# Kernel tuning notes

Measured on AMD Instinct MI355X. Metric: run time of the kernel, lower is better.

The kernel has to match this reference:

```python
import math
import jax, jax.numpy as jnp
import numpy as np

T_STEPS = 128       # number of diffusion 'experts'
BASE = 64
CH = BASE * 2       # 128 working channels
TE = 256            # time embedding dim
B, IN_C, H, W = 8, 3, 128, 128
EPS = 1e-5


def _conv(x, w, b):
    # x: [N,C,H,W], w: [O,I,3,3] (or 1x1)
    y = jax.lax.conv_general_dilated(x, w, (1, 1), 'SAME',
                                     dimension_numbers=('NCHW', 'OIHW', 'NCHW'))
    return y + b[None, :, None, None]


def _gn(x, scale, bias, groups=8):
    n, c, h, w = x.shape
    xg = x.reshape(n, groups, c // groups, h, w)
    m = xg.mean((2, 3, 4), keepdims=True)
    v = xg.var((2, 3, 4), keepdims=True)
    xn = ((xg - m) * jax.lax.rsqrt(v + EPS)).reshape(n, c, h, w)
    return xn * scale[None, :, None, None] + bias[None, :, None, None]


def setup_inputs() -> dict:
    key = jax.random.key(0)
    ks = iter(jax.random.split(key, 64))
    def p(shape, s=0.05):
        return jax.random.normal(next(ks), shape, jnp.float32) * s
    return {
        'x': jax.random.normal(next(ks), (B, IN_C, H, W), jnp.float32),
        't': jax.random.randint(next(ks), (B,), 0, T_STEPS),
        # feature_extraction
        'fe_w1': p((BASE, IN_C, 3, 3)), 'fe_b1': jnp.zeros((BASE,), jnp.float32),
        'fe_g1s': jnp.ones((BASE,), jnp.float32), 'fe_g1b': jnp.zeros((BASE,), jnp.float32),
        'fe_w2': p((CH, BASE, 3, 3)), 'fe_b2': jnp.zeros((CH,), jnp.float32),
        'fe_g2s': jnp.ones((CH,), jnp.float32), 'fe_g2b': jnp.zeros((CH,), jnp.float32),
        # stacked per-step expert params [T, ...]
        'mlp_w1': p((T_STEPS, TE, TE)), 'mlp_b1': jnp.zeros((T_STEPS, TE), jnp.float32),
        'mlp_w2': p((T_STEPS, CH, TE)), 'mlp_b2': jnp.zeros((T_STEPS, CH), jnp.float32),
        'c1w': p((T_STEPS, CH, CH + 1, 3, 3)), 'c1b': jnp.zeros((T_STEPS, CH), jnp.float32),
        'g1s': jnp.ones((T_STEPS, CH), jnp.float32), 'g1b': jnp.zeros((T_STEPS, CH), jnp.float32),
        'c2w': p((T_STEPS, CH, CH, 3, 3)), 'c2b': jnp.zeros((T_STEPS, CH), jnp.float32),
        'g2s': jnp.ones((T_STEPS, CH), jnp.float32), 'g2b': jnp.zeros((T_STEPS, CH), jnp.float32),
        'c3w': p((T_STEPS, CH, CH, 3, 3)), 'c3b': jnp.zeros((T_STEPS, CH), jnp.float32),
        # color_reconstruction
        'cr_w1': p((BASE, CH, 3, 3)), 'cr_b1': jnp.zeros((BASE,), jnp.float32),
        'cr_gs': jnp.ones((BASE,), jnp.float32), 'cr_gb': jnp.zeros((BASE,), jnp.float32),
        'cr_w2': p((IN_C, BASE, 3, 3)), 'cr_b2': jnp.zeros((IN_C,), jnp.float32),
        # weight_generator (1x1 conv on pooled features)
        'wg_w': p((1, CH, 1, 1)), 'wg_b': jnp.zeros((1,), jnp.float32),
    }


def _expert(xi, tei, w1, b1, w2, b2, cw1, cb1, gs1, gb1, cw2, cb2, gs2, gb2, cw3, cb3):
    # Single-sample DiffusionStep. xi: [C,H,W], tei: [TE]
    h = jax.nn.silu(w1 @ tei + b1)
    tc = (w2 @ h + b2).mean()  # scalar time channel (fix of original view(-1,1,1,1) bug)
    xb = xi[None]  # [1,C,H,W]
    tmap = jnp.broadcast_to(tc, (1, 1) + xi.shape[1:])
    z = jnp.concatenate([xb, tmap], axis=1)  # [1,C+1,H,W]
    z = jax.nn.silu(_gn(_conv(z, cw1, cb1), gs1, gb1))
    z = jax.nn.silu(_gn(_conv(z, cw2, cb2), gs2, gb2))
    z = _conv(z, cw3, cb3)
    return z[0]


def _forward(x, t, fe_w1, fe_b1, fe_g1s, fe_g1b, fe_w2, fe_b2, fe_g2s, fe_g2b,
             mlp_w1, mlp_b1, mlp_w2, mlp_b2, c1w, c1b, g1s, g1b,
             c2w, c2b, g2s, g2b, c3w, c3b,
             cr_w1, cr_b1, cr_gs, cr_gb, cr_w2, cr_b2, wg_w, wg_b):
    feat = jax.nn.silu(_gn(_conv(x, fe_w1, fe_b1), fe_g1s, fe_g1b))
    feat = jax.nn.silu(_gn(_conv(feat, fe_w2, fe_b2), fe_g2s, fe_g2b))  # [B,CH,H,W]

    # sinusoidal time embedding
    half = TE // 2
    freqs = jnp.exp(jnp.arange(half, dtype=jnp.float32) * (-math.log(10000.0) / (half - 1)))
    e = t.astype(jnp.float32)[:, None] * freqs[None, :]
    temb = jnp.concatenate([jnp.sin(e), jnp.cos(e)], axis=-1)  # [B,TE]

    # Each sample matches exactly one step: gather its expert weights, apply once.
    g = lambda a: jnp.take(a, t, axis=0)
    noise = jax.vmap(_expert)(feat, temb,
                              g(mlp_w1), g(mlp_b1), g(mlp_w2), g(mlp_b2),
                              g(c1w), g(c1b), g(g1s), g(g1b),
                              g(c2w), g(c2b), g(g2s), g(g2b),
                              g(c3w), g(c3b))
    alpha = 1.0 - t.astype(jnp.float32) / T_STEPS
    x_t = feat - alpha[:, None, None, None] * noise

    r = jax.nn.silu(_gn(_conv(x_t, cr_w1, cr_b1), cr_gs, cr_gb))
    restored = jax.nn.sigmoid(_conv(r, cr_w2, cr_b2))  # [B,3,H,W]

    pooled = x_t.mean((2, 3))  # adaptive avg pool to 1x1 -> [B,CH]
    weight = jax.nn.sigmoid(pooled @ wg_w[:, :, 0, 0].T + wg_b)[:, :, None, None]  # [B,1,1,1]
    return restored, weight


def reference(x, t, fe_w1, fe_b1, fe_g1s, fe_g1b, fe_w2, fe_b2, fe_g2s, fe_g2b,
              mlp_w1, mlp_b1, mlp_w2, mlp_b2, c1w, c1b, g1s, g1b,
              c2w, c2b, g2s, g2b, c3w, c3b,
              cr_w1, cr_b1, cr_gs, cr_gb, cr_w2, cr_b2, wg_w, wg_b):
    return _forward(x, t, fe_w1, fe_b1, fe_g1s, fe_g1b, fe_w2, fe_b2, fe_g2s, fe_g2b,
                    mlp_w1, mlp_b1, mlp_w2, mlp_b2, c1w, c1b, g1s, g1b,
                    c2w, c2b, g2s, g2b, c3w, c3b,
                    cr_w1, cr_b1, cr_gs, cr_gb, cr_w2, cr_b2, wg_w, wg_b)
```

## Files before the change

kernel.cpp:

```cpp
#include <hip/hip_runtime.h>
#include <hip/hip_bf16.h>

typedef __hip_bfloat16 bf16;

#define HW 128
#define IMG 16384
#define EPSV 1e-5f

typedef __bf16 b16x8 __attribute__((ext_vector_type(8)));
typedef float f32x16 __attribute__((ext_vector_type(16)));

__device__ __forceinline__ float u2f(unsigned int u){ union{unsigned int i; float f;}c; c.i=u; return c.f; }
__device__ __forceinline__ float blo(unsigned int u){ return u2f(u<<16); }
__device__ __forceinline__ float bhi(unsigned int u){ return u2f(u & 0xffff0000u); }
__device__ __forceinline__ unsigned short f2bu(float v){ bf16 h=__float2bfloat16(v); union{bf16 b; unsigned short s;}c; c.b=h; return c.s; }
__device__ __forceinline__ unsigned int pk(float a, float b){ return (unsigned int)f2bu(a) | ((unsigned int)f2bu(b)<<16); }
__device__ __forceinline__ bf16 f2b(float v){ return __float2bfloat16(v); }
__device__ __forceinline__ float sigm(float x){ return 1.f/(1.f+__expf(-x)); }

__device__ __forceinline__ void gload16(const void* g, void* l) {
    __builtin_amdgcn_global_load_lds((const __attribute__((address_space(1))) unsigned int*)(g),
                                     (__attribute__((address_space(3))) unsigned int*)(l), 16, 0, 0);
}

__device__ __forceinline__ f32x16 MFMA(b16x8 a, b16x8 b, f32x16 c){
    return __builtin_amdgcn_mfma_f32_32x32x16_bf16(a, b, c, 0, 0, 0);
}

template<int CIN, int COUT, bool TADD>
__global__ void __launch_bounds__(256, 2)
mfma_conv3x3(const bf16* __restrict__ act,
             const bf16* __restrict__ Wt,
             const float* __restrict__ Bt,
             bf16* __restrict__ outp,
             const float* __restrict__ Tt,
             const bf16* __restrict__ zerobuf)
{
    static_assert(CIN==64 || CIN==128, "");
    static_assert(COUT==64 || COUT==128, "");
    constexpr int NT = COUT/64;
    constexpr int XB_ROW = 136*128;
    constexpr int XB_BYTES = 2*XB_ROW;
    constexpr int WA_BYTES = COUT*128;
    __shared__ char smem[XB_BYTES + WA_BYTES];
    char* Xb = smem;
    char* Wa = smem + XB_BYTES;

    const int n    = blockIdx.z;
    const int tile = blockIdx.x;
    const int y0   = tile*2;
    const int tid  = threadIdx.x;
    const int lane = tid & 63;
    const int wid  = tid >> 6;
    const int wm   = wid >> 1;
    const int wn   = wid & 1;
    const int l31  = lane & 31;
    const int lhi  = lane >> 5;

    const bf16* actN = act + (size_t)n * IMG * CIN;
    const bf16* WtN  = Wt  + (size_t)n * 9 * COUT * CIN;

    f32x16 acc[4][NT];
    #pragma unroll
    for (int i=0;i<4;++i)
        #pragma unroll
        for (int j=0;j<NT;++j)
            #pragma unroll
            for (int k=0;k<16;++k) acc[i][j][k] = 0.f;

    for (int dy = 0; dy < 3; ++dy) {
        for (int ch = 0; ch < CIN/64; ++ch) {
            for (int u = wid; u < 34; u += 4) {
                int row  = (u >= 17) ? 1 : 0;
                int j    = u - row*17;
                int slot = j*64 + lane;
                int xp = slot >> 3, g = slot & 7;
                int x  = xp - 1;
                int ry = y0 + dy - 1 + row;
                const void* src;
                if ((unsigned)x < 128u && (unsigned)ry < 128u)
                    src = actN + ((size_t)(ry*128 + x)*CIN + ch*64 + 8*(g ^ (xp&7)));
                else
                    src = zerobuf;
                gload16(src, Xb + row*XB_ROW + j*1024);
            }
            for (int dx = 0; dx < 3; ++dx) {
                int r = dy*3 + dx;
                for (int u = wid; u < COUT/8; u += 4) {
                    int co = u*8 + (lane>>3), g = lane & 7;
                    const void* src = WtN + ((size_t)(r*COUT + co)*CIN + ch*64 + 8*(g ^ (co&7)));
                    gload16(src, Wa + u*1024);
                }
                __syncthreads();
                #pragma unroll
                for (int s = 0; s < 4; ++s) {
                    int koff = s*32 + lhi*16;
                    b16x8 bfr[NT];
                    #pragma unroll
                    for (int q = 0; q < NT; ++q) {
                        int co = wn*32*NT + q*32 + l31;
                        bfr[q] = *(const b16x8*)(Wa + co*128 + (koff ^ ((co&7)<<4)));
                    }
                    b16x8 afr[4];
                    #pragma unroll
                    for (int mt = 0; mt < 4; ++mt) {
                        int xp = mt*32 + l31 + dx;
                        afr[mt] = *(const b16x8*)(Xb + wm*XB_ROW + xp*128 + (koff ^ ((xp&7)<<4)));
                    }
                    #pragma unroll
                    for (int mt = 0; mt < 4; ++mt)
                        #pragma unroll
                        for (int q = 0; q < NT; ++q)
                            acc[mt][q] = MFMA(afr[mt], bfr[q], acc[mt][q]);
                }
                __syncthreads();
            }
        }
    }

    const float* BtN = Bt + n*COUT;
    const int y = y0 + wm;
    bf16* outRow = outp + ((size_t)n*IMG + (size_t)y*128)*COUT;
    #pragma unroll
    for (int q = 0; q < NT; ++q) {
        int co = wn*32*NT + q*32 + l31;
        float bv = BtN[co];
        float T0=0.f, T1=0.f, T2=0.f;
        if (TADD) {
            int yt = (y==0) ? 0 : (y==127 ? 2 : 1);
            const float* Tp = Tt + (size_t)(n*COUT + co)*9 + yt*3;
            T0 = Tp[0]; T1 = Tp[1]; T2 = Tp[2];
        }
        #pragma unroll
        for (int mt = 0; mt < 4; ++mt) {
            #pragma unroll
            for (int reg = 0; reg < 16; ++reg) {
                int x = mt*32 + (reg&3) + 8*(reg>>2) + 4*lhi;
                float v = acc[mt][q][reg] + bv;
                if (TADD) v += (x==0) ? T0 : (x==127 ? T2 : T1);
                outRow[(size_t)x*COUT + co] = f2b(v);
            }
        }
    }
}

__global__ void __launch_bounds__(256)
wtprep_kernel(const float* __restrict__ w, const float* __restrict__ b,
              const int* __restrict__ t, bf16* __restrict__ Wt, float* __restrict__ Bt,
              int CO, int COsrc, int CIN, int CINW, int gather)
{
    int idx = blockIdx.x*256 + threadIdx.x;
    int total = 8*9*CO*CIN;
    if (idx >= total) return;
    int cin = idx & (CIN-1);
    int tmp = idx / CIN;
    int co  = tmp % CO;
    int tmp2 = tmp / CO;
    int r   = tmp2 % 9;
    int n   = tmp2 / 9;
    int sel = gather ? t[n] : 0;
    float v = 0.f;
    if (co < COsrc) v = w[(((size_t)sel*COsrc + co)*CINW + cin)*9 + r];
    Wt[idx] = f2b(v);
    if (cin==0 && r==0) Bt[n*CO+co] = (co < COsrc) ? b[(size_t)sel*COsrc + co] : 0.f;
}

__global__ void __launch_bounds__(256)
tprep_kernel(const int* __restrict__ t, const float* __restrict__ c1w,
             const float* __restrict__ tc, float* __restrict__ Tt)
{
    int idx = blockIdx.x*256 + threadIdx.x;
    if (idx >= 8*128) return;
    int n = idx >> 7, co = idx & 127;
    const float* wp = c1w + ((size_t)t[n]*128 + co)*129*9 + 128*9;
    float w9[9];
    #pragma unroll
    for (int i=0;i<9;++i) w9[i] = wp[i];
    float tcv = tc[n];
    #pragma unroll
    for (int yt=0; yt<3; ++yt)
        #pragma unroll
        for (int xt=0; xt<3; ++xt) {
            float s = 0.f;
            #pragma unroll
            for (int dy=0; dy<3; ++dy)
                #pragma unroll
                for (int dx=0; dx<3; ++dx) {
                    bool vy = (yt==0) ? (dy>=1) : ((yt==2) ? (dy<=1) : true);
                    bool vx = (xt==0) ? (dx>=1) : ((xt==2) ? (dx<=1) : true);
                    if (vy && vx) s += w9[dy*3+dx];
                }
            Tt[(size_t)idx*9 + yt*3+xt] = tcv*s;
        }
}

__global__ void __launch_bounds__(256)
fe1_kernel(const float* __restrict__ in, const float* __restrict__ w,
           const float* __restrict__ bias, bf16* __restrict__ out)
{
    const int n   = blockIdx.z;
    const int co0 = blockIdx.y * 8;
    const int tx0 = (blockIdx.x & 7) * 16;
    const int ty0 = (blockIdx.x >> 3) * 16;
    const int lx = threadIdx.x & 15, ly = threadIdx.x >> 4;
    __shared__ float tileS[18][19];
    float acc[8];
    #pragma unroll
    for (int i=0;i<8;++i) acc[i] = bias[co0+i];
    const float* inN = in + (size_t)n*3*IMG;
    for (int ci=0; ci<3; ++ci) {
        __syncthreads();
        for (int idx = threadIdx.x; idx < 18*18; idx += 256) {
            int tyy = idx/18, txx = idx - tyy*18;
            int gy = ty0+tyy-1, gx = tx0+txx-1;
            float v = 0.f;
            if ((unsigned)gy < 128u && (unsigned)gx < 128u) v = inN[ci*IMG + gy*128+gx];
            tileS[tyy][txx] = v;
        }
        __syncthreads();
        float v[9];
        #pragma unroll
        for (int ky=0;ky<3;++ky)
            #pragma unroll
            for (int kx=0;kx<3;++kx) v[ky*3+kx] = tileS[ly+ky][lx+kx];
        #pragma unroll
        for (int c=0;c<8;++c) {
            const float* wp = w + ((co0+c)*3 + ci)*9;
            #pragma unroll
            for (int k=0;k<9;++k) acc[c] = fmaf(v[k], wp[k], acc[c]);
        }
    }
    int gy = ty0+ly, gx = tx0+lx;
    uint4 o; o.x = pk(acc[0],acc[1]); o.y = pk(acc[2],acc[3]);
    o.z = pk(acc[4],acc[5]); o.w = pk(acc[6],acc[7]);
    *(uint4*)(out + ((size_t)n*IMG + gy*128+gx)*64 + co0) = o;
}

template<int C>
__global__ void __launch_bounds__(256)
gn_stats_nhwc(const bf16* __restrict__ x, float* __restrict__ partials)
{
    constexpr int L2CPG = (C==128) ? 4 : 3;
    const int chunk = blockIdx.x, n = blockIdx.y;
    const int t = threadIdx.x;
    const uint4* pv = (const uint4*)(x + ((size_t)n*IMG + chunk*256 + t)*C);
    float s[8], ss[8];
    #pragma unroll
    for (int g=0; g<8; ++g) { s[g]=0.f; ss[g]=0.f; }
    #pragma unroll
    for (int v=0; v<C/8; ++v) {
        int g = (v*8) >> L2CPG;
        uint4 u = pv[v];
        float f0=blo(u.x), f1=bhi(u.x), f2=blo(u.y), f3=bhi(u.y);
        float f4=blo(u.z), f5=bhi(u.z), f6=blo(u.w), f7=bhi(u.w);
        s[g]  += ((f0+f1)+(f2+f3)) + ((f4+f5)+(f6+f7));
        ss[g] += ((f0*f0+f1*f1)+(f2*f2+f3*f3)) + ((f4*f4+f5*f5)+(f6*f6+f7*f7));
    }
    __shared__ float sh[16][256];
    #pragma unroll
    for (int g=0; g<8; ++g) { sh[2*g][t] = s[g]; sh[2*g+1][t] = ss[g]; }
    __syncthreads();
    for (int off=128; off>0; off>>=1) {
        if (t < off) {
            #pragma unroll
            for (int k=0;k<16;++k) sh[k][t] += sh[k][t+off];
        }
        __syncthreads();
    }
    if (t < 16) partials[((size_t)n*64 + chunk)*16 + t] = sh[t][0];
}

__global__ void __launch_bounds__(128)
gn_final(const float* __restrict__ partials, const float* __restrict__ scale,
         const float* __restrict__ bias, const int* __restrict__ tsel,
         int C, int l2cpg, float* __restrict__ scA, float* __restrict__ biA)
{
    int n = blockIdx.x, c = threadIdx.x;
    if (c >= C) return;
    int g = c >> l2cpg;
    float s=0.f, ss=0.f;
    for (int k=0;k<64;++k) {
        s  += partials[((size_t)n*64+k)*16 + 2*g];
        ss += partials[((size_t)n*64+k)*16 + 2*g + 1];
    }
    float cnt = (float)IMG * (float)(C>>3);
    float m = s/cnt, var = ss/cnt - m*m;
    float r = rsqrtf(var + EPSV);
    int po = tsel ? tsel[n]*C : 0;
    float sc = scale[po+c]*r;
    scA[n*C+c] = sc;
    biA[n*C+c] = bias[po+c] - m*sc;
}

template<int C>
__global__ void __launch_bounds__(256)
gn_apply_nhwc(bf16* __restrict__ x, const float* __restrict__ scA, const float* __restrict__ biA)
{
    size_t e0 = ((size_t)blockIdx.x*256 + threadIdx.x)*8;
    int n = (int)(e0 >> ((C==128) ? 21 : 20));
    int c0 = (int)(e0 & (C-1));
    const float4 sA = *(const float4*)(scA + n*C + c0);
    const float4 sB = *(const float4*)(scA + n*C + c0 + 4);
    const float4 bA = *(const float4*)(biA + n*C + c0);
    const float4 bB = *(const float4*)(biA + n*C + c0 + 4);
    uint4* p = (uint4*)(x + e0);
    uint4 u = *p;
    float f[8] = {blo(u.x),bhi(u.x),blo(u.y),bhi(u.y),blo(u.z),bhi(u.z),blo(u.w),bhi(u.w)};
    f[0]=f[0]*sA.x+bA.x; f[1]=f[1]*sA.y+bA.y; f[2]=f[2]*sA.z+bA.z; f[3]=f[3]*sA.w+bA.w;
    f[4]=f[4]*sB.x+bB.x; f[5]=f[5]*sB.y+bB.y; f[6]=f[6]*sB.z+bB.z; f[7]=f[7]*sB.w+bB.w;
    #pragma unroll
    for (int i=0;i<8;++i) f[i] = f[i]*sigm(f[i]);
    u.x = pk(f[0],f[1]); u.y = pk(f[2],f[3]); u.z = pk(f[4],f[5]); u.w = pk(f[6],f[7]);
    *p = u;
}

__global__ void __launch_bounds__(256)
time_mlp_kernel(const int* __restrict__ t,
                const float* __restrict__ w1, const float* __restrict__ b1,
                const float* __restrict__ w2, const float* __restrict__ b2,
                float* __restrict__ tc)
{
    const int n = blockIdx.x;
    const int ti = t[n];
    const int tid = threadIdx.x;
    __shared__ float temb[256];
    __shared__ float h[256];
    {
        int j = tid & 127;
        float fr = expf(-9.210340371976184f / 127.f * (float)j);
        float e = (float)ti * fr;
        temb[tid] = (tid < 128) ? sinf(e) : cosf(e);
    }
    __syncthreads();
    {
        const float* w1p = w1 + ((size_t)ti * 256 + tid) * 256;
        float s = b1[(size_t)ti * 256 + tid];
        for (int j = 0; j < 256; ++j) s += w1p[j] * temb[j];
        h[tid] = s * sigm(s);
    }
    __syncthreads();
    float part = 0.f;
    if (tid < 128) {
        const float* w2p = w2 + ((size_t)ti * 128 + tid) * 256;
        float s = b2[(size_t)ti * 128 + tid];
        for (int j = 0; j < 256; ++j) s += w2p[j] * h[j];
        part = s;
    }
    __shared__ float red[256];
    red[tid] = part;
    __syncthreads();
    for (int off = 128; off > 0; off >>= 1) {
        if (tid < off) red[tid] += red[tid + off];
        __syncthreads();
    }
    if (tid == 0) tc[n] = red[0] * (1.f / 128.f);
}

__global__ void __launch_bounds__(256)
xt_pool_nhwc(bf16* __restrict__ feat, const bf16* __restrict__ noise,
             const int* __restrict__ t, const float* __restrict__ wgw,
             float* __restrict__ partials)
{
    size_t e0 = ((size_t)blockIdx.x*256 + threadIdx.x)*8;
    int n = (int)(e0 >> 21);
    int c0 = (int)(e0 & 127);
    float alpha = 1.f - (float)t[n] * (1.f / 128.f);
    const float4 wA = *(const float4*)(wgw + c0);
    const float4 wB = *(const float4*)(wgw + c0 + 4);
    uint4 f = *(const uint4*)(feat + e0);
    uint4 z = *(const uint4*)(noise + e0);
    float xf[8] = {blo(f.x),bhi(f.x),blo(f.y),bhi(f.y),blo(f.z),bhi(f.z),blo(f.w),bhi(f.w)};
    float xz[8] = {blo(z.x),bhi(z.x),blo(z.y),bhi(z.y),blo(z.z),bhi(z.z),blo(z.w),bhi(z.w)};
    float wv[8] = {wA.x,wA.y,wA.z,wA.w,wB.x,wB.y,wB.z,wB.w};
    float s = 0.f;
    #pragma unroll
    for (int i=0;i<8;++i) { float v = xf[i] - alpha*xz[i]; xf[i] = v; s += v*wv[i]; }
    uint4 o;
    o.x = pk(xf[0],xf[1]); o.y = pk(xf[2],xf[3]); o.z = pk(xf[4],xf[5]); o.w = pk(xf[6],xf[7]);
    *(uint4*)(feat + e0) = o;
    __shared__ float sh[256];
    sh[threadIdx.x] = s;
    __syncthreads();
    for (int off = 128; off > 0; off >>= 1) {
        if ((int)threadIdx.x < off) sh[threadIdx.x] += sh[threadIdx.x + off];
        __syncthreads();
    }
    if (threadIdx.x == 0) partials[blockIdx.x] = sh[0];
}

__global__ void __launch_bounds__(256)
weight_final_kernel(const float* __restrict__ partials, const float* __restrict__ wg_b,
                    float* __restrict__ outw)
{
    const int n = blockIdx.x;
    float s = 0.f;
    for (int i = threadIdx.x; i < 1024; i += 256) s += partials[n * 1024 + i];
    __shared__ float sh[256];
    sh[threadIdx.x] = s;
    __syncthreads();
    for (int off = 128; off > 0; off >>= 1) {
        if ((int)threadIdx.x < off) sh[threadIdx.x] += sh[threadIdx.x + off];
        __syncthreads();
    }
    if (threadIdx.x == 0) {
        float w = sh[0] * (1.f / 16384.f) + wg_b[0];
        outw[n] = sigm(w);
    }
}

__global__ void __launch_bounds__(256)
extract_kernel(const bf16* __restrict__ in, float* __restrict__ out)
{
    int n = blockIdx.y;
    int px = blockIdx.x*256 + threadIdx.x;
    const bf16* p = in + ((size_t)n*IMG + px)*64;
    float r0 = __bfloat162float(p[0]);
    float r1 = __bfloat162float(p[1]);
    float r2 = __bfloat162float(p[2]);
    size_t ob = (size_t)n*3*IMG + px;
    out[ob]         = sigm(r0);
    out[ob + IMG]   = sigm(r1);
    out[ob + 2*IMG] = sigm(r2);
}

extern "C" void kernel_launch(void* const* d_in, const int* in_sizes, int n_in,
                              void* d_out, int out_size, void* d_ws, size_t ws_size,
                              hipStream_t stream)
{
    (void)in_sizes; (void)n_in; (void)out_size; (void)ws_size;

    const float* x      = (const float*)d_in[0];
    const int*   t      = (const int*)  d_in[1];
    const float* fe_w1  = (const float*)d_in[2];
    const float* fe_b1  = (const float*)d_in[3];
    const float* fe_g1s = (const float*)d_in[4];
    const float* fe_g1b = (const float*)d_in[5];
    const float* fe_w2  = (const float*)d_in[6];
    const float* fe_b2  = (const float*)d_in[7];
    const float* fe_g2s = (const float*)d_in[8];
    const float* fe_g2b = (const float*)d_in[9];
    const float* mlp_w1 = (const float*)d_in[10];
    const float* mlp_b1 = (const float*)d_in[11];
    const float* mlp_w2 = (const float*)d_in[12];
    const float* mlp_b2 = (const float*)d_in[13];
    const float* c1w    = (const float*)d_in[14];
    const float* c1b    = (const float*)d_in[15];
    const float* g1s    = (const float*)d_in[16];
    const float* g1b    = (const float*)d_in[17];
    const float* c2w    = (const float*)d_in[18];
    const float* c2b    = (const float*)d_in[19];
    const float* g2s    = (const float*)d_in[20];
    const float* g2b    = (const float*)d_in[21];
    const float* c3w    = (const float*)d_in[22];
    const float* c3b    = (const float*)d_in[23];
    const float* cr_w1  = (const float*)d_in[24];
    const float* cr_b1  = (const float*)d_in[25];
    const float* cr_gs  = (const float*)d_in[26];
    const float* cr_gb  = (const float*)d_in[27];
    const float* cr_w2  = (const float*)d_in[28];
    const float* cr_b2  = (const float*)d_in[29];
    const float* wg_w   = (const float*)d_in[30];
    const float* wg_b   = (const float*)d_in[31];

    char* ws = (char*)d_ws;
    bf16* A   = (bf16*)(ws);
    bf16* Bb  = (bf16*)(ws + 33554432);
    bf16* Cb  = (bf16*)(ws + 67108864);
    bf16* Wt  = (bf16*)(ws + 100663296);
    float* Bt = (float*)(ws + 103022592);
    float* Tt = (float*)(ws + 103026688);
    float* tc = (float*)(ws + 103063552);
    bf16* zb  = (bf16*)(ws + 103063616);
    float* gp = (float*)(ws + 103063680);
    float* scA = (float*)(ws + 103096448);
    float* biA = (float*)(ws + 103100544);
    float* wp  = (float*)(ws + 103104640);

    float* out_img = (float*)d_out;
    float* out_w   = out_img + 393216;

    dim3 blk(256);
    hipMemsetAsync(zb, 0, 64, stream);

    time_mlp_kernel<<<8, blk, 0, stream>>>(t, mlp_w1, mlp_b1, mlp_w2, mlp_b2, tc);
    tprep_kernel<<<4, blk, 0, stream>>>(t, c1w, tc, Tt);

    fe1_kernel<<<dim3(64, 8, 8), blk, 0, stream>>>(x, fe_w1, fe_b1, Bb);
    gn_stats_nhwc<64><<<dim3(64, 8), blk, 0, stream>>>(Bb, gp);
    gn_final<<<8, 128, 0, stream>>>(gp, fe_g1s, fe_g1b, nullptr, 64, 3, scA, biA);
    gn_apply_nhwc<64><<<4096, blk, 0, stream>>>(Bb, scA, biA);

    wtprep_kernel<<<2304, blk, 0, stream>>>(fe_w2, fe_b2, t, Wt, Bt, 128, 128, 64, 64, 0);
    mfma_conv3x3<64,128,false><<<dim3(64, 1, 8), blk, 0, stream>>>(Bb, Wt, Bt, A, nullptr, zb);
    gn_stats_nhwc<128><<<dim3(64, 8), blk, 0, stream>>>(A, gp);
    gn_final<<<8, 128, 0, stream>>>(gp, fe_g2s, fe_g2b, nullptr, 128, 4, scA, biA);
    gn_apply_nhwc<128><<<8192, blk, 0, stream>>>(A, scA, biA);

    wtprep_kernel<<<4608, blk, 0, stream>>>(c1w, c1b, t, Wt, Bt, 128, 128, 128, 129, 1);
    mfma_conv3x3<128,128,true><<<dim3(64, 1, 8), blk, 0, stream>>>(A, Wt, Bt, Bb, Tt, zb);
    gn_stats_nhwc<128><<<dim3(64, 8), blk, 0, stream>>>(Bb, gp);
    gn_final<<<8, 128, 0, stream>>>(gp, g1s, g1b, t, 128, 4, scA, biA);
    gn_apply_nhwc<128><<<8192, blk, 0, stream>>>(Bb, scA, biA);

    wtprep_kernel<<<4608, blk, 0, stream>>>(c2w, c2b, t, Wt, Bt, 128, 128, 128, 128, 1);
    mfma_conv3x3<128,128,false><<<dim3(64, 1, 8), blk, 0, stream>>>(Bb, Wt, Bt, Cb, nullptr, zb);
    gn_stats_nhwc<128><<<dim3(64, 8), blk, 0, stream>>>(Cb, gp);
    gn_final<<<8, 128, 0, stream>>>(gp, g2s, g2b, t, 128, 4, scA, biA);
    gn_apply_nhwc<128><<<8192, blk, 0, stream>>>(Cb, scA, biA);

    wtprep_kernel<<<4608, blk, 0, stream>>>(c3w, c3b, t, Wt, Bt, 128, 128, 128, 128, 1);
    mfma_conv3x3<128,128,false><<<dim3(64, 1, 8), blk, 0, stream>>>(Cb, Wt, Bt, Bb, nullptr, zb);

    xt_pool_nhwc<<<8192, blk, 0, stream>>>(A, Bb, t, wg_w, wp);
    weight_final_kernel<<<8, blk, 0, stream>>>(wp, wg_b, out_w);

    wtprep_kernel<<<2304, blk, 0, stream>>>(cr_w1, cr_b1, t, Wt, Bt, 64, 64, 128, 128, 0);
    mfma_conv3x3<128,64,false><<<dim3(64, 1, 8), blk, 0, stream>>>(A, Wt, Bt, Cb, nullptr, zb);
    gn_stats_nhwc<64><<<dim3(64, 8), blk, 0, stream>>>(Cb, gp);
    gn_final<<<8, 128, 0, stream>>>(gp, cr_gs, cr_gb, nullptr, 64, 3, scA, biA);
    gn_apply_nhwc<64><<<4096, blk, 0, stream>>>(Cb, scA, biA);

    wtprep_kernel<<<1152, blk, 0, stream>>>(cr_w2, cr_b2, t, Wt, Bt, 64, 3, 64, 64, 0);
    mfma_conv3x3<64,64,false><<<dim3(64, 1, 8), blk, 0, stream>>>(Cb, Wt, Bt, Bb, nullptr, zb);
    extract_kernel<<<dim3(64, 8), blk, 0, stream>>>(Bb, out_img);
}
```

Before: 443.8 us.

## Fuse GroupNorm stats and x_t/pool into conv epilogue, double-buffer weight staging

Each conv kernel now accumulates per-group sum and sum-of-squares in its epilogue and writes per-tile partials, which removes the separate gn_stats passes. The final expert conv computes x_t = feat - alpha*noise and the gating dot product in its epilogue, which removes the xt_pool kernel. The conv main loop is restructured to double-buffer weight tiles so the next tap's weights are prefetched while MFMA runs, with a compact input row layout and a raised wave priority during MFMA. The fused epilogues add register pressure and extra syncs, and the GN partial layout must still match what gn_final expects.

```diff
diff --git a/kernel.cpp b/kernel.cpp
--- a/kernel.cpp
+++ b/kernel.cpp
@@ -27,24 +27,31 @@
     return __builtin_amdgcn_mfma_f32_32x32x16_bf16(a, b, c, 0, 0, 0);
 }
 
-template<int CIN, int COUT, bool TADD>
+template<int CIN, int COUT, bool TADD, bool FUSE_GN, bool FUSE_XT>
 __global__ void __launch_bounds__(256, 2)
 mfma_conv3x3(const bf16* __restrict__ act,
              const bf16* __restrict__ Wt,
              const float* __restrict__ Bt,
              bf16* __restrict__ outp,
              const float* __restrict__ Tt,
-             const bf16* __restrict__ zerobuf)
+             const bf16* __restrict__ zerobuf,
+             float* __restrict__ gpart,
+             const bf16* __restrict__ featA,
+             const int* __restrict__ tsel,
+             const float* __restrict__ wgw,
+             float* __restrict__ wpart)
 {
     static_assert(CIN==64 || CIN==128, "");
     static_assert(COUT==64 || COUT==128, "");
-    constexpr int NT = COUT/64;
-    constexpr int XB_ROW = 136*128;
-    constexpr int XB_BYTES = 2*XB_ROW;
-    constexpr int WA_BYTES = COUT*128;
-    __shared__ char smem[XB_BYTES + WA_BYTES];
-    char* Xb = smem;
-    char* Wa = smem + XB_BYTES;
+    constexpr int NT  = COUT/64;
+    constexpr int CH  = CIN/64;
+    constexpr int P   = 9*CH;
+    constexpr int WCH = COUT/8;
+    constexpr int WSZ = WCH*1024;
+
+    __shared__ char Xb[33792];
+    __shared__ char Wa[2][WSZ];
+    __shared__ float redS[4][4], redSS[4][4], redW[4];
 
     const int n    = blockIdx.z;
     const int tile = blockIdx.x;
@@ -68,63 +75,107 @@
             #pragma unroll
             for (int k=0;k<16;++k) acc[i][j][k] = 0.f;
 
-    for (int dy = 0; dy < 3; ++dy) {
-        for (int ch = 0; ch < CIN/64; ++ch) {
-            for (int u = wid; u < 34; u += 4) {
-                int row  = (u >= 17) ? 1 : 0;
-                int j    = u - row*17;
-                int slot = j*64 + lane;
-                int xp = slot >> 3, g = slot & 7;
-                int x  = xp - 1;
-                int ry = y0 + dy - 1 + row;
-                const void* src;
-                if ((unsigned)x < 128u && (unsigned)ry < 128u)
-                    src = actN + ((size_t)(ry*128 + x)*CIN + ch*64 + 8*(g ^ (xp&7)));
-                else
-                    src = zerobuf;
-                gload16(src, Xb + row*XB_ROW + j*1024);
+    auto stage_X = [&](int dy, int ch) {
+        const int ry0 = y0 + dy - 1;
+        for (int u = wid; u < 33; u += 4) {
+            int s = u*8 + (lane>>3);
+            int g = lane & 7;
+            int r  = (s >= 130) ? 1 : 0;
+            int xp = s - r*130;
+            int xx = xp - 1;
+            int ry = ry0 + r;
+            const void* src = zerobuf;
+            if (s < 260 && (unsigned)xx < 128u && (unsigned)ry < 128u)
+                src = actN + ((size_t)(ry*128 + xx)*CIN + ch*64 + 8*(g ^ (s&7)));
+            gload16(src, Xb + u*1024);
+        }
+    };
+    auto stage_W = [&](int r, int ch, int buf) {
+        for (int u = wid; u < WCH; u += 4) {
+            int co = u*8 + (lane>>3);
+            int g  = lane & 7;
+            const void* src = WtN + ((size_t)(r*COUT + co)*CIN + ch*64 + 8*(g ^ (co&7)));
+            gload16(src, Wa[buf] + u*1024);
+        }
+    };
+
+    stage_X(0, 0);
+    stage_W(0, 0, 0);
+    __syncthreads();
+
+    int buf = 0;
+    for (int p = 0; p < P; ++p) {
+        const int dx = p % 3;
+        const int pc = p / 3;
+        const int ch = pc % CH;
+        const int dy = pc / CH;
+        const bool last = (p+1 == P);
+
+        if (!last) {
+            const int pn  = p + 1;
+            const int ndx = pn % 3;
+            const int npc = pn / 3;
+            const int nch = npc % CH;
+            const int ndy = npc / CH;
+            stage_W(ndy*3 + ndx, nch, buf ^ 1);
+        }
+        (void)dy; (void)ch;
+
+        __builtin_amdgcn_s_setprio(1);
+        #pragma unroll
+        for (int s = 0; s < 4; ++s) {
+            const int koff = s*32 + lhi*16;
+            b16x8 bfr[NT];
+            #pragma unroll
+            for (int q = 0; q < NT; ++q) {
+                int co = wn*32*NT + q*32 + l31;
+                bfr[q] = *(const b16x8*)(Wa[buf] + co*128 + (koff ^ ((co&7)<<4)));
             }
-            for (int dx = 0; dx < 3; ++dx) {
-                int r = dy*3 + dx;
-                for (int u = wid; u < COUT/8; u += 4) {
-                    int co = u*8 + (lane>>3), g = lane & 7;
-                    const void* src = WtN + ((size_t)(r*COUT + co)*CIN + ch*64 + 8*(g ^ (co&7)));
-                    gload16(src, Wa + u*1024);
-                }
+            b16x8 afr[4];
+            #pragma unroll
+            for (int mt = 0; mt < 4; ++mt) {
+                int sl = wm*130 + mt*32 + l31 + dx;
+                afr[mt] = *(const b16x8*)(Xb + sl*128 + (koff ^ ((sl&7)<<4)));
+            }
+            #pragma unroll
+            for (int mt = 0; mt < 4; ++mt)
+                #pragma unroll
+                for (int q = 0; q < NT; ++q)
+                    acc[mt][q] = MFMA(afr[mt], bfr[q], acc[mt][q]);
+        }
+        __builtin_amdgcn_s_setprio(0);
+
+        if (!last) {
+            if (dx == 2) {
                 __syncthreads();
-                #pragma unroll
-                for (int s = 0; s < 4; ++s) {
-                    int koff = s*32 + lhi*16;
-                    b16x8 bfr[NT];
-                    #pragma unroll
-                    for (int q = 0; q < NT; ++q) {
-                        int co = wn*32*NT + q*32 + l31;
-                        bfr[q] = *(const b16x8*)(Wa + co*128 + (koff ^ ((co&7)<<4)));
-                    }
-                    b16x8 afr[4];
-                    #pragma unroll
-                    for (int mt = 0; mt < 4; ++mt) {
-                        int xp = mt*32 + l31 + dx;
-                        afr[mt] = *(const b16x8*)(Xb + wm*XB_ROW + xp*128 + (koff ^ ((xp&7)<<4)));
-                    }
-                    #pragma unroll
-                    for (int mt = 0; mt < 4; ++mt)
-                        #pragma unroll
-                        for (int q = 0; q < NT; ++q)
-                            acc[mt][q] = MFMA(afr[mt], bfr[q], acc[mt][q]);
-                }
+                const int pn  = p + 1;
+                const int npc = pn / 3;
+                stage_X(npc / CH, npc % CH);
+                __syncthreads();
+            } else {
                 __syncthreads();
             }
         }
+        buf ^= 1;
     }
 
     const float* BtN = Bt + n*COUT;
     const int y = y0 + wm;
     bf16* outRow = outp + ((size_t)n*IMG + (size_t)y*128)*COUT;
+    const bf16* featRow = FUSE_XT ? (featA + ((size_t)n*IMG + (size_t)y*128)*COUT) : nullptr;
+    float alpha = 0.f;
+    if (FUSE_XT) alpha = 1.f - (float)tsel[n] * (1.f/128.f);
+
+    float gs[NT], gss[NT], wsum = 0.f;
+    #pragma unroll
+    for (int q = 0; q < NT; ++q) { gs[q]=0.f; gss[q]=0.f; }
+
     #pragma unroll
     for (int q = 0; q < NT; ++q) {
-        int co = wn*32*NT + q*32 + l31;
-        float bv = BtN[co];
+        const int co = wn*32*NT + q*32 + l31;
+        const float bv = BtN[co];
+        float wg = 0.f;
+        if (FUSE_XT) wg = wgw[co];
         float T0=0.f, T1=0.f, T2=0.f;
         if (TADD) {
             int yt = (y==0) ? 0 : (y==127 ? 2 : 1);
@@ -135,12 +186,52 @@
         for (int mt = 0; mt < 4; ++mt) {
             #pragma unroll
             for (int reg = 0; reg < 16; ++reg) {
-                int x = mt*32 + (reg&3) + 8*(reg>>2) + 4*lhi;
+                const int x = mt*32 + (reg&3) + 8*(reg>>2) + 4*lhi;
                 float v = acc[mt][q][reg] + bv;
                 if (TADD) v += (x==0) ? T0 : (x==127 ? T2 : T1);
-                outRow[(size_t)x*COUT + co] = f2b(v);
+                if (FUSE_GN) { gs[q] += v; gss[q] += v*v; }
+                if (FUSE_XT) {
+                    float fv = __bfloat162float(featRow[(size_t)x*COUT + co]);
+                    float xt = fv - alpha*v;
+                    outRow[(size_t)x*COUT + co] = f2b(xt);
+                    wsum += xt * wg;
+                } else {
+                    outRow[(size_t)x*COUT + co] = f2b(v);
+                }
             }
         }
+    }
+
+    if (FUSE_GN) {
+        constexpr int LG = (COUT==128) ? 4 : 3;
+        #pragma unroll
+        for (int q = 0; q < NT; ++q) {
+            float a = gs[q], b = gss[q];
+            #pragma unroll
+            for (int m = 1; m < (1<<LG); m <<= 1) { a += __shfl_xor(a, m); b += __shfl_xor(b, m); }
+            a += __shfl_xor(a, 32); b += __shfl_xor(b, 32);
+            const int co = wn*32*NT + q*32 + l31;
+            if (lhi == 0 && (l31 & ((1<<LG)-1)) == 0) {
+                int j = (co >> LG) & 3;
+                redS[wid][j] = a; redSS[wid][j] = b;
+            }
+        }
+        __syncthreads();
+        if (tid < 8) {
+            int g = tid, wn_ = g>>2, j = g&3;
+            float S  = redS[wn_][j]  + redS[2+wn_][j];
+            float SS = redSS[wn_][j] + redSS[2+wn_][j];
+            gpart[((size_t)(n*64 + tile))*16 + 2*g]     = S;
+            gpart[((size_t)(n*64 + tile))*16 + 2*g + 1] = SS;
+        }
+    }
+    if (FUSE_XT) {
+        float a = wsum;
+        #pragma unroll
+        for (int m = 1; m < 64; m <<= 1) a += __shfl_xor(a, m);
+        if (lane == 0) redW[wid] = a;
+        __syncthreads();
+        if (tid == 0) wpart[n*64 + tile] = redW[0]+redW[1]+redW[2]+redW[3];
     }
 }
 
@@ -356,56 +447,15 @@
     if (tid == 0) tc[n] = red[0] * (1.f / 128.f);
 }
 
-__global__ void __launch_bounds__(256)
-xt_pool_nhwc(bf16* __restrict__ feat, const bf16* __restrict__ noise,
-             const int* __restrict__ t, const float* __restrict__ wgw,
-             float* __restrict__ partials)
-{
-    size_t e0 = ((size_t)blockIdx.x*256 + threadIdx.x)*8;
-    int n = (int)(e0 >> 21);
-    int c0 = (int)(e0 & 127);
-    float alpha = 1.f - (float)t[n] * (1.f / 128.f);
-    const float4 wA = *(const float4*)(wgw + c0);
-    const float4 wB = *(const float4*)(wgw + c0 + 4);
-    uint4 f = *(const uint4*)(feat + e0);
-    uint4 z = *(const uint4*)(noise + e0);
-    float xf[8] = {blo(f.x),bhi(f.x),blo(f.y),bhi(f.y),blo(f.z),bhi(f.z),blo(f.w),bhi(f.w)};
-    float xz[8] = {blo(z.x),bhi(z.x),blo(z.y),bhi(z.y),blo(z.z),bhi(z.z),blo(z.w),bhi(z.w)};
-    float wv[8] = {wA.x,wA.y,wA.z,wA.w,wB.x,wB.y,wB.z,wB.w};
-    float s = 0.f;
-    #pragma unroll
-    for (int i=0;i<8;++i) { float v = xf[i] - alpha*xz[i]; xf[i] = v; s += v*wv[i]; }
-    uint4 o;
-    o.x = pk(xf[0],xf[1]); o.y = pk(xf[2],xf[3]); o.z = pk(xf[4],xf[5]); o.w = pk(xf[6],xf[7]);
-    *(uint4*)(feat + e0) = o;
-    __shared__ float sh[256];
-    sh[threadIdx.x] = s;
-    __syncthreads();
-    for (int off = 128; off > 0; off >>= 1) {
-        if ((int)threadIdx.x < off) sh[threadIdx.x] += sh[threadIdx.x + off];
-        __syncthreads();
-    }
-    if (threadIdx.x == 0) partials[blockIdx.x] = sh[0];
-}
-
-__global__ void __launch_bounds__(256)
-weight_final_kernel(const float* __restrict__ partials, const float* __restrict__ wg_b,
+__global__ void __launch_bounds__(64)
+weight_final_kernel(const float* __restrict__ wpart, const float* __restrict__ wg_b,
                     float* __restrict__ outw)
 {
     const int n = blockIdx.x;
-    float s = 0.f;
-    for (int i = threadIdx.x; i < 1024; i += 256) s += partials[n * 1024 + i];
-    __shared__ float sh[256];
-    sh[threadIdx.x] = s;
-    __syncthreads();
-    for (int off = 128; off > 0; off >>= 1) {
-        if ((int)threadIdx.x < off) sh[threadIdx.x] += sh[threadIdx.x + off];
-        __syncthreads();
-    }
-    if (threadIdx.x == 0) {
-        float w = sh[0] * (1.f / 16384.f) + wg_b[0];
-        outw[n] = sigm(w);
-    }
+    float s = wpart[n*64 + threadIdx.x];
+    #pragma unroll
+    for (int m = 1; m < 64; m <<= 1) s += __shfl_xor(s, m);
+    if (threadIdx.x == 0) outw[n] = sigm(s * (1.f/16384.f) + wg_b[0]);
 }
 
 __global__ void __launch_bounds__(256)
@@ -480,6 +530,7 @@
     float* out_w   = out_img + 393216;
 
     dim3 blk(256);
+    dim3 cgrid(64, 1, 8);
     hipMemsetAsync(zb, 0, 64, stream);
 
     time_mlp_kernel<<<8, blk, 0, stream>>>(t, mlp_w1, mlp_b1, mlp_w2, mlp_b2, tc);
@@ -491,36 +542,30 @@
     gn_apply_nhwc<64><<<4096, blk, 0, stream>>>(Bb, scA, biA);
 
     wtprep_kernel<<<2304, blk, 0, stream>>>(fe_w2, fe_b2, t, Wt, Bt, 128, 128, 64, 64, 0);
-    mfma_conv3x3<64,128,false><<<dim3(64, 1, 8), blk, 0, stream>>>(Bb, Wt, Bt, A, nullptr, zb);
-    gn_stats_nhwc<128><<<dim3(64, 8), blk, 0, stream>>>(A, gp);
+    mfma_conv3x3<64,128,false,true,false><<<cgrid, blk, 0, stream>>>(Bb, Wt, Bt, A, nullptr, zb, gp, nullptr, nullptr, nullptr, nullptr);
     gn_final<<<8, 128, 0, stream>>>(gp, fe_g2s, fe_g2b, nullptr, 128, 4, scA, biA);
     gn_apply_nhwc<128><<<8192, blk, 0, stream>>>(A, scA, biA);
 
     wtprep_kernel<<<4608, blk, 0, stream>>>(c1w, c1b, t, Wt, Bt, 128, 128, 128, 129, 1);
-    mfma_conv3x3<128,128,true><<<dim3(64, 1, 8), blk, 0, stream>>>(A, Wt, Bt, Bb, Tt, zb);
-    gn_stats_nhwc<128><<<dim3(64, 8), blk, 0, stream>>>(Bb, gp);
+    mfma_conv3x3<128,128,true,true,false><<<cgrid, blk, 0, stream>>>(A, Wt, Bt, Bb, Tt, zb, gp, nullptr, nullptr, nullptr, nullptr);
     gn_final<<<8, 128, 0, stream>>>(gp, g1s, g1b, t, 128, 4, scA, biA);
     gn_apply_nhwc<128><<<8192, blk, 0, stream>>>(Bb, scA, biA);
 
     wtprep_kernel<<<4608, blk, 0, stream>>>(c2w, c2b, t, Wt, Bt, 128, 128, 128, 128, 1);
-    mfma_conv3x3<128,128,false><<<dim3(64, 1, 8), blk, 0, stream>>>(Bb, Wt, Bt, Cb, nullptr, zb);
-    gn_stats_nhwc<128><<<dim3(64, 8), blk, 0, stream>>>(Cb, gp);
+    mfma_conv3x3<128,128,false,true,false><<<cgrid, blk, 0, stream>>>(Bb, Wt, Bt, Cb, nullptr, zb, gp, nullptr, nullptr, nullptr, nullptr);
     gn_final<<<8, 128, 0, stream>>>(gp, g2s, g2b, t, 128, 4, scA, biA);
     gn_apply_nhwc<128><<<8192, blk, 0, stream>>>(Cb, scA, biA);
 
     wtprep_kernel<<<4608, blk, 0, stream>>>(c3w, c3b, t, Wt, Bt, 128, 128, 128, 128, 1);
-    mfma_conv3x3<128,128,false><<<dim3(64, 1, 8), blk, 0, stream>>>(Cb, Wt, Bt, Bb, nullptr, zb);
-
-    xt_pool_nhwc<<<8192, blk, 0, stream>>>(A, Bb, t, wg_w, wp);
-    weight_final_kernel<<<8, blk, 0, stream>>>(wp, wg_b, out_w);
+    mfma_conv3x3<128,128,false,false,true><<<cgrid, blk, 0, stream>>>(Cb, Wt, Bt, Bb, nullptr, zb, nullptr, A, t, wg_w, wp);
+    weight_final_kernel<<<8, 64, 0, stream>>>(wp, wg_b, out_w);
 
     wtprep_kernel<<<2304, blk, 0, stream>>>(cr_w1, cr_b1, t, Wt, Bt, 64, 64, 128, 128, 0);
-    mfma_conv3x3<128,64,false><<<dim3(64, 1, 8), blk, 0, stream>>>(A, Wt, Bt, Cb, nullptr, zb);
-    gn_stats_nhwc<64><<<dim3(64, 8), blk, 0, stream>>>(Cb, gp);
+    mfma_conv3x3<128,64,false,true,false><<<cgrid, blk, 0, stream>>>(Bb, Wt, Bt, Cb, nullptr, zb, gp, nullptr, nullptr, nullptr, nullptr);
     gn_final<<<8, 128, 0, stream>>>(gp, cr_gs, cr_gb, nullptr, 64, 3, scA, biA);
     gn_apply_nhwc<64><<<4096, blk, 0, stream>>>(Cb, scA, biA);
 
     wtprep_kernel<<<1152, blk, 0, stream>>>(cr_w2, cr_b2, t, Wt, Bt, 64, 3, 64, 64, 0);
-    mfma_conv3x3<64,64,false><<<dim3(64, 1, 8), blk, 0, stream>>>(Cb, Wt, Bt, Bb, nullptr, zb);
-    extract_kernel<<<dim3(64, 8), blk, 0, stream>>>(Bb, out_img);
-}
+    mfma_conv3x3<64,64,false,false,false><<<cgrid, blk, 0, stream>>>(Cb, Wt, Bt, A, nullptr, zb, nullptr, nullptr, nullptr, nullptr, nullptr);
+    extract_kernel<<<dim3(64, 8), blk, 0, stream>>>(A, out_img);
+}
```

New measurement: 375.7 us. -15.3%, faster.
